# Performance work log

Hardware: AMD Instinct MI355X
Metric: run time of the kernel (lower is better)

The kernel has to match this reference:

```python
import jax, jax.numpy as jnp
import numpy as np

EPS = 1e-6


def setup_inputs() -> dict:
    key = jax.random.key(0)
    k1, k2, k3, k4 = jax.random.split(key, 4)
    B, L, H, E = 16, 4096, 8, 64
    return {
        "queries": jax.random.normal(k1, (B, L, H, E), dtype=jnp.float32),
        "keys": jax.random.normal(k2, (B, L, H, E), dtype=jnp.float32),
        "values": jax.random.normal(k3, (B, L, H, E), dtype=jnp.float32),
        "attn_mask": jnp.ones((1,), dtype=bool),
        "gamma": jax.random.uniform(k4, (1,), dtype=jnp.float32),
    }


def reference(queries, keys, values, attn_mask, gamma):
    # Faithful to the original: keys/values/attn_mask are unused; Q=K=V=queries.
    B, L, H, E = queries.shape
    HE = H * E
    V = queries.reshape(B, L, HE)              # raw values [B, L, HE]
    # l2_norm: normalize over dim=-2 (the L axis)
    Qn = V / jnp.linalg.norm(V, axis=-2, keepdims=True)   # [B, L, HE]
    Kt = jnp.swapaxes(Qn, -1, -2)              # K = l2_norm(K).permute -> [B, HE, L]
    # tailor_sum: 1 / (HE + sum_n Kt[b,n,l] * (sum_l' Qn[b,l',n] + eps))  -> [B, L]
    q_colsum = jnp.sum(Qn, axis=-2) + EPS      # [B, HE]
    tailor = 1.0 / (HE + jnp.einsum('bnl,bn->bl', Kt, q_colsum))  # [B, L]
    # value_sum over L, broadcast to [B, L, HE]
    value_sum = jnp.sum(V, axis=-2)            # [B, HE]
    # (V @ K) @ Q == V @ (K @ Q): use the linear-complexity [HE,HE] inner matrix
    KQ = jnp.einsum('bnl,blm->bnm', Kt, Qn)    # [B, HE, HE]
    part = jnp.einsum('bln,bnm->blm', V, KQ)   # [B, L, HE]
    matrix_sum = value_sum[:, None, :] + part  # [B, L, HE]
    weight_value = (matrix_sum * tailor[:, :, None]).reshape(B, L, H, E)
    return queries + gamma * weight_value
```

## Files before the change

### kernel.cpp

```cpp
#include <hip/hip_runtime.h>

#define EPS 1e-6f
#define LL 4096
#define HE 512

typedef __attribute__((ext_vector_type(8))) short short8;
typedef __attribute__((ext_vector_type(4))) float f32x4;

__device__ __forceinline__ unsigned short f2bf(float f) {
    union { float f; unsigned u; } v; v.f = f;
    unsigned r = v.u + 0x7FFFu + ((v.u >> 16) & 1u);
    return (unsigned short)(r >> 16);
}
__device__ __forceinline__ float bf2f(unsigned short s) {
    union { unsigned u; float f; } v; v.u = ((unsigned)s) << 16;
    return v.f;
}
__device__ __forceinline__ void gl16(const unsigned short* g, unsigned short* l) {
    __builtin_amdgcn_global_load_lds(
        (const __attribute__((address_space(1))) unsigned int*)(const void*)g,
        (__attribute__((address_space(3))) unsigned int*)(void*)l,
        16, 0, 0);
}

__global__ __launch_bounds__(256) void k1_fused(const float* __restrict__ q,
        unsigned short* __restrict__ Vt, unsigned short* __restrict__ Vb,
        float* __restrict__ ps, float* __restrict__ pq, int bofs, int pstride) {
    __shared__ unsigned short lds[64][65];
    int blk = blockIdx.x;
    int b = blk >> 9, lt = (blk >> 3) & 63, nt = blk & 7;
    int gb = bofs + b;
    int t = threadIdx.x;
    int row = t >> 4, col = (t & 15) << 2;
    const float* base = q + ((size_t)gb * LL + lt * 64) * HE + nt * 64;
    unsigned short* vbb = Vb + ((size_t)b * LL + lt * 64) * HE + nt * 64;
    #pragma unroll
    for (int i = 0; i < 4; i++) {
        int l = row + i * 16;
        float4 v = *(const float4*)(base + (size_t)l * HE + col);
        ushort4 w;
        w.x = f2bf(v.x); w.y = f2bf(v.y); w.z = f2bf(v.z); w.w = f2bf(v.w);
        lds[col+0][l] = w.x; lds[col+1][l] = w.y;
        lds[col+2][l] = w.z; lds[col+3][l] = w.w;
        *(ushort4*)(vbb + (size_t)l * HE + col) = w;
    }
    __syncthreads();
    unsigned short* ob = Vt + ((size_t)b * HE + nt * 64) * LL + lt * 64;
    #pragma unroll
    for (int i = 0; i < 4; i++) {
        int n = row + i * 16;
        ushort4 w;
        w.x = lds[n][col+0]; w.y = lds[n][col+1];
        w.z = lds[n][col+2]; w.w = lds[n][col+3];
        *(ushort4*)(ob + (size_t)n * LL + col) = w;
        float x0 = bf2f(w.x), x1 = bf2f(w.y), x2 = bf2f(w.z), x3 = bf2f(w.w);
        float s = x0 + x1 + x2 + x3;
        float qq = x0*x0 + x1*x1 + x2*x2 + x3*x3;
        s += __shfl_xor(s, 1);  qq += __shfl_xor(qq, 1);
        s += __shfl_xor(s, 2);  qq += __shfl_xor(qq, 2);
        s += __shfl_xor(s, 4);  qq += __shfl_xor(qq, 4);
        s += __shfl_xor(s, 8);  qq += __shfl_xor(qq, 8);
        if ((t & 15) == 0) {
            int idx = lt * pstride + b * 512 + nt * 64 + n;
            ps[idx] = s;
            pq[idx] = qq;
        }
    }
}

__global__ __launch_bounds__(256) void k2_reduce(const float* __restrict__ ps,
        const float* __restrict__ pq, float* __restrict__ sumV,
        float* __restrict__ cvec, float* __restrict__ invn, int bofs, int pstride) {
    int i = blockIdx.x * 256 + threadIdx.x;
    float s = 0.f, qq = 0.f;
    #pragma unroll 8
    for (int lt = 0; lt < 64; lt++) {
        s  += ps[(size_t)lt * pstride + i];
        qq += pq[(size_t)lt * pstride + i];
    }
    int o = bofs * HE + i;
    float inv = 1.0f / sqrtf(qq);
    sumV[o] = s;
    invn[o] = inv;
    cvec[o] = (s * inv + EPS) * inv;
}

__global__ __launch_bounds__(256) void k3_dvec(const unsigned short* __restrict__ Vb,
        const float* __restrict__ cvec, float* __restrict__ dvec, int bofs) {
    int blk = blockIdx.x;
    int b = blk >> 7, lblk = blk & 127;
    int t = threadIdx.x;
    int lloc = t >> 3, j = t & 7;
    int l = lblk * 32 + lloc;
    const unsigned short* rowp = Vb + ((size_t)b * LL + l) * HE + j * 64;
    const float* cp = cvec + (bofs + b) * HE + j * 64;
    float d = 0.f;
    #pragma unroll
    for (int g = 0; g < 8; g++) {
        short8 v = *(const short8*)(rowp + g * 8);
        float4 c0 = *(const float4*)(cp + g * 8);
        float4 c1 = *(const float4*)(cp + g * 8 + 4);
        d += bf2f((unsigned short)v[0]) * c0.x + bf2f((unsigned short)v[1]) * c0.y
           + bf2f((unsigned short)v[2]) * c0.z + bf2f((unsigned short)v[3]) * c0.w
           + bf2f((unsigned short)v[4]) * c1.x + bf2f((unsigned short)v[5]) * c1.y
           + bf2f((unsigned short)v[6]) * c1.z + bf2f((unsigned short)v[7]) * c1.w;
    }
    d += __shfl_xor(d, 1); d += __shfl_xor(d, 2); d += __shfl_xor(d, 4);
    if (j == 0) dvec[(size_t)(bofs + b) * LL + l] = d;
}

__global__ __launch_bounds__(256) void k4_gram(const unsigned short* __restrict__ Vt,
        unsigned short* __restrict__ Gp) {
    __shared__ __attribute__((aligned(16))) unsigned short la[128][64];
    __shared__ __attribute__((aligned(16))) unsigned short lb[128][64];
    int cpx = gridDim.x >> 3;
    int blk = ((int)blockIdx.x & 7) * cpx + ((int)blockIdx.x >> 3);
    int b = blk / 80;
    int rem = blk - b * 80;
    int pair = rem >> 3, split = rem & 7;
    int nt = (pair < 4) ? 0 : (pair < 7) ? 1 : (pair < 9) ? 2 : 3;
    int off = (nt * (9 - nt)) >> 1;
    int mt = nt + pair - off;
    bool diag = (nt == mt);
    int N0 = nt * 128, M0 = mt * 128;
    int t = threadIdx.x;
    int w = t >> 6, lane = t & 63;
    int wr = w >> 1, wc = w & 1;
    int rl = lane >> 3;
    int cl = ((lane & 7) ^ rl) << 3;
    int lr = lane & 15, q4 = lane >> 4;
    int ch0 = (q4 ^ (lane & 7)) << 3;
    const unsigned short* pa = Vt + ((size_t)b * HE + N0) * LL + split * 512;
    const unsigned short* pb = Vt + ((size_t)b * HE + M0) * LL + split * 512;
    const unsigned short (*LB)[64] = diag ? la : lb;
    f32x4 acc[4][4] = {};
    for (int kb = 0; kb < 8; kb++) {
        int k0 = kb * 64;
        #pragma unroll
        for (int p = 0; p < 4; p++) {
            int r0 = p * 32 + w * 8;
            gl16(pa + (size_t)(r0 + rl) * LL + k0 + cl, &la[r0][0]);
            if (!diag) gl16(pb + (size_t)(r0 + rl) * LL + k0 + cl, &lb[r0][0]);
        }
        __syncthreads();
        #pragma unroll
        for (int ks = 0; ks < 2; ks++) {
            int colA = ch0 ^ (ks << 5);
            short8 af[4], bfr[4];
            #pragma unroll
            for (int i = 0; i < 4; i++)
                af[i] = *(const short8*)&la[wr*64 + i*16 + lr][colA];
            #pragma unroll
            for (int j = 0; j < 4; j++)
                bfr[j] = *(const short8*)&LB[wc*64 + j*16 + lr][colA];
            #pragma unroll
            for (int i = 0; i < 4; i++)
                #pragma unroll
                for (int j = 0; j < 4; j++)
                    acc[i][j] = __builtin_amdgcn_mfma_f32_16x16x32_bf16(af[i], bfr[j], acc[i][j], 0, 0, 0);
        }
        __syncthreads();
    }
    size_t tbase = ((size_t)(b * 10 + pair) * 8 + split) * 16384;
    #pragma unroll
    for (int i = 0; i < 4; i++) {
        int nb = wr*64 + i*16 + q4*4;
        #pragma unroll
        for (int j = 0; j < 4; j++) {
            int ml = wc*64 + j*16 + lr;
            ushort4 wv;
            wv.x = f2bf(acc[i][j][0]); wv.y = f2bf(acc[i][j][1]);
            wv.z = f2bf(acc[i][j][2]); wv.w = f2bf(acc[i][j][3]);
            *(ushort4*)&Gp[tbase + (size_t)ml * 128 + nb] = wv;
        }
    }
}

__global__ __launch_bounds__(256) void k5_reduce(const unsigned short* __restrict__ Gp,
        const float* __restrict__ invn, unsigned short* __restrict__ KQb, int bofs) {
    __shared__ unsigned short lds_t[128][130];
    int blk = blockIdx.x;
    int b = blk / 10, pair = blk % 10;
    int nt = (pair < 4) ? 0 : (pair < 7) ? 1 : (pair < 9) ? 2 : 3;
    int off = (nt * (9 - nt)) >> 1;
    int mt = nt + pair - off;
    int N0 = nt * 128, M0 = mt * 128;
    int t = threadIdx.x;
    const unsigned short* gp = Gp + ((size_t)(b * 10 + pair) * 8) * 16384;
    const float* inb = invn + (size_t)(bofs + b) * HE;
    #pragma unroll 2
    for (int e = 0; e < 32; e++) {
        int idx = e * 512 + t * 2;
        int ml = idx >> 7, nl = idx & 127;
        float s0 = 0.f, s1 = 0.f;
        #pragma unroll
        for (int sp = 0; sp < 8; sp++) {
            unsigned g2 = *(const unsigned*)&gp[(size_t)sp * 16384 + idx];
            s0 += bf2f((unsigned short)(g2 & 0xFFFF));
            s1 += bf2f((unsigned short)(g2 >> 16));
        }
        float im = inb[M0 + ml];
        ushort2 v;
        v.x = f2bf(s0 * inb[N0 + nl] * im);
        v.y = f2bf(s1 * inb[N0 + nl + 1] * im);
        *(ushort2*)&KQb[((size_t)b * HE + M0 + ml) * HE + N0 + nl] = v;
        *(ushort2*)&lds_t[ml][nl] = v;
    }
    __syncthreads();
    #pragma unroll 2
    for (int e = 0; e < 32; e++) {
        int idx = e * 512 + t * 2;
        int nl = idx >> 7, ml = idx & 127;
        ushort2 v;
        v.x = lds_t[ml][nl];
        v.y = lds_t[ml + 1][nl];
        *(ushort2*)&KQb[((size_t)b * HE + N0 + nl) * HE + M0 + ml] = v;
    }
}

__global__ __launch_bounds__(256) void k6_part(const unsigned short* __restrict__ KQb,
        const unsigned short* __restrict__ Vb, const float* __restrict__ dvec,
        const float* __restrict__ sumV, const float* __restrict__ gamma,
        float* __restrict__ out, int bofs) {
    __shared__ __attribute__((aligned(16))) unsigned short la[128][64];
    __shared__ __attribute__((aligned(16))) unsigned short lb[128][64];
    int cpx = gridDim.x >> 3;
    int blk = ((int)blockIdx.x & 7) * cpx + ((int)blockIdx.x >> 3);
    int b = blk >> 7, mt = (blk >> 5) & 3, lt = blk & 31;
    int gb = bofs + b;
    int M0 = mt * 128, L0 = lt * 128;
    int t = threadIdx.x;
    int w = t >> 6, lane = t & 63;
    int wr = w >> 1, wc = w & 1;
    int rl = lane >> 3;
    int cl = ((lane & 7) ^ rl) << 3;
    int lr = lane & 15, q4 = lane >> 4;
    int ch0 = (q4 ^ (lane & 7)) << 3;
    const unsigned short* pa = KQb + ((size_t)b * HE + M0) * HE;
    const unsigned short* pb = Vb + ((size_t)b * LL + L0) * HE;
    f32x4 acc[4][4] = {};
    for (int kb = 0; kb < 8; kb++) {
        int k0 = kb * 64;
        #pragma unroll
        for (int p = 0; p < 4; p++) {
            int r0 = p * 32 + w * 8;
            gl16(pa + (size_t)(r0 + rl) * HE + k0 + cl, &la[r0][0]);
            gl16(pb + (size_t)(r0 + rl) * HE + k0 + cl, &lb[r0][0]);
        }
        __syncthreads();
        #pragma unroll
        for (int ks = 0; ks < 2; ks++) {
            int colA = ch0 ^ (ks << 5);
            short8 af[4], bfr[4];
            #pragma unroll
            for (int i = 0; i < 4; i++)
                af[i] = *(const short8*)&la[wr*64 + i*16 + lr][colA];
            #pragma unroll
            for (int j = 0; j < 4; j++)
                bfr[j] = *(const short8*)&lb[wc*64 + j*16 + lr][colA];
            #pragma unroll
            for (int i = 0; i < 4; i++)
                #pragma unroll
                for (int j = 0; j < 4; j++)
                    acc[i][j] = __builtin_amdgcn_mfma_f32_16x16x32_bf16(af[i], bfr[j], acc[i][j], 0, 0, 0);
        }
        __syncthreads();
    }
    float gma = gamma[0];
    #pragma unroll
    for (int j = 0; j < 4; j++) {
        int lglob = L0 + wc*64 + j*16 + lr;
        float dt = dvec[(size_t)gb * LL + lglob];
        float tailor = 1.0f / (512.0f + dt);
        #pragma unroll
        for (int i = 0; i < 4; i++) {
            int m4 = M0 + wr*64 + i*16 + q4*4;
            size_t ofs = ((size_t)gb * LL + lglob) * HE + m4;
            ushort4 rv = *(const ushort4*)(Vb + ((size_t)b * LL + lglob) * HE + m4);
            float4 vs = *(const float4*)(sumV + (size_t)gb * HE + m4);
            float4 o;
            o.x = bf2f(rv.x) + gma * (vs.x + acc[i][j][0]) * tailor;
            o.y = bf2f(rv.y) + gma * (vs.y + acc[i][j][1]) * tailor;
            o.z = bf2f(rv.z) + gma * (vs.z + acc[i][j][2]) * tailor;
            o.w = bf2f(rv.w) + gma * (vs.w + acc[i][j][3]) * tailor;
            *(float4*)(out + ofs) = o;
        }
    }
}

extern "C" void kernel_launch(void* const* d_in, const int* in_sizes, int n_in,
                              void* d_out, int out_size, void* d_ws, size_t ws_size,
                              hipStream_t stream) {
    const float* q     = (const float*)d_in[0];
    const float* gamma = (const float*)d_in[4];
    float* out = (float*)d_out;
    char* ws = (char*)d_ws;
    float* sumV  = (float*)(ws);
    float* cvec  = (float*)(ws + 65536);
    float* invn  = (float*)(ws + 98304);
    float* dvec  = (float*)(ws + 131072);

    if (ws_size >= 190000000ull) {
        unsigned short* KQb = (unsigned short*)(ws + 524288);
        unsigned short* Vt  = (unsigned short*)(ws + 8912896);
        unsigned short* Vb  = (unsigned short*)(ws + 76021760);
        unsigned short* Gp  = (unsigned short*)(ws + 143130624);
        float* ps = (float*)(ws + 185073664);
        float* pq = (float*)(ws + 187170816);
        k1_fused <<<8192, 256, 0, stream>>>(q, Vt, Vb, ps, pq, 0, 8192);
        k2_reduce<<<32,   256, 0, stream>>>(ps, pq, sumV, cvec, invn, 0, 8192);
        k3_dvec  <<<2048, 256, 0, stream>>>(Vb, cvec, dvec, 0);
        k4_gram  <<<1280, 256, 0, stream>>>(Vt, Gp);
        k5_reduce<<<160,  256, 0, stream>>>(Gp, invn, KQb, 0);
        k6_part  <<<2048, 256, 0, stream>>>(KQb, Vb, dvec, sumV, gamma, out, 0);
    } else {
        unsigned short* KQb = (unsigned short*)(ws + 524288);
        unsigned short* Vt  = (unsigned short*)(ws + 524288 + 4194304);
        unsigned short* Vb  = (unsigned short*)(ws + 524288 + 4194304 + 33554432);
        unsigned short* Gp = (unsigned short*)((float*)d_out + 16777216);
        float* ps = (float*)d_out + 22020096;
        float* pq = ps + 262144;
        for (int h = 0; h < 2; h++) {
            int bofs = h * 8;
            k1_fused <<<4096, 256, 0, stream>>>(q, Vt, Vb, ps, pq, bofs, 4096);
            k2_reduce<<<16,   256, 0, stream>>>(ps, pq, sumV, cvec, invn, bofs, 4096);
            k3_dvec  <<<1024, 256, 0, stream>>>(Vb, cvec, dvec, bofs);
            k4_gram  <<<640,  256, 0, stream>>>(Vt, Gp);
            k5_reduce<<<80,   256, 0, stream>>>(Gp, invn, KQb, bofs);
            k6_part  <<<1024, 256, 0, stream>>>(KQb, Vb, dvec, sumV, gamma, out, bofs);
        }
    }
}
```

Before: 210.5 us.

## Double-buffer LDS tiles in gram and part GEMM kernels

After: 199.5 us. 5.2% less time.

```diff
diff --git a/kernel.cpp b/kernel.cpp
--- a/kernel.cpp
+++ b/kernel.cpp
@@ -111,8 +111,8 @@
 
 __global__ __launch_bounds__(256) void k4_gram(const unsigned short* __restrict__ Vt,
         unsigned short* __restrict__ Gp) {
-    __shared__ __attribute__((aligned(16))) unsigned short la[128][64];
-    __shared__ __attribute__((aligned(16))) unsigned short lb[128][64];
+    __shared__ __attribute__((aligned(16))) unsigned short la[2][128][64];
+    __shared__ __attribute__((aligned(16))) unsigned short lb[2][128][64];
     int cpx = gridDim.x >> 3;
     int blk = ((int)blockIdx.x & 7) * cpx + ((int)blockIdx.x >> 3);
     int b = blk / 80;
@@ -132,35 +132,50 @@
     int ch0 = (q4 ^ (lane & 7)) << 3;
     const unsigned short* pa = Vt + ((size_t)b * HE + N0) * LL + split * 512;
     const unsigned short* pb = Vt + ((size_t)b * HE + M0) * LL + split * 512;
-    const unsigned short (*LB)[64] = diag ? la : lb;
     f32x4 acc[4][4] = {};
+
+#define STAGE4(B, KB) do { \
+    int _k0 = (KB) * 64; \
+    _Pragma("unroll") \
+    for (int p = 0; p < 4; p++) { \
+        int r0 = p * 32 + w * 8; \
+        gl16(pa + (size_t)(r0 + rl) * LL + _k0 + cl, &la[B][r0][0]); \
+        if (!diag) gl16(pb + (size_t)(r0 + rl) * LL + _k0 + cl, &lb[B][r0][0]); \
+    } } while (0)
+
+    STAGE4(0, 0);
+    #pragma unroll
     for (int kb = 0; kb < 8; kb++) {
-        int k0 = kb * 64;
-        #pragma unroll
-        for (int p = 0; p < 4; p++) {
-            int r0 = p * 32 + w * 8;
-            gl16(pa + (size_t)(r0 + rl) * LL + k0 + cl, &la[r0][0]);
-            if (!diag) gl16(pb + (size_t)(r0 + rl) * LL + k0 + cl, &lb[r0][0]);
-        }
-        __syncthreads();
+        int cur = kb & 1;
+        if (kb < 7) {
+            STAGE4(cur ^ 1, kb + 1);
+            if (diag) { asm volatile("s_waitcnt vmcnt(4)" ::: "memory"); }
+            else      { asm volatile("s_waitcnt vmcnt(8)" ::: "memory"); }
+        } else {
+            asm volatile("s_waitcnt vmcnt(0)" ::: "memory");
+        }
+        __builtin_amdgcn_s_barrier();
+        const unsigned short (*A)[64] = la[cur];
+        const unsigned short (*Bp)[64] = diag ? la[cur] : lb[cur];
         #pragma unroll
         for (int ks = 0; ks < 2; ks++) {
             int colA = ch0 ^ (ks << 5);
             short8 af[4], bfr[4];
             #pragma unroll
             for (int i = 0; i < 4; i++)
-                af[i] = *(const short8*)&la[wr*64 + i*16 + lr][colA];
+                af[i] = *(const short8*)&A[wr*64 + i*16 + lr][colA];
             #pragma unroll
             for (int j = 0; j < 4; j++)
-                bfr[j] = *(const short8*)&LB[wc*64 + j*16 + lr][colA];
+                bfr[j] = *(const short8*)&Bp[wc*64 + j*16 + lr][colA];
             #pragma unroll
             for (int i = 0; i < 4; i++)
                 #pragma unroll
                 for (int j = 0; j < 4; j++)
                     acc[i][j] = __builtin_amdgcn_mfma_f32_16x16x32_bf16(af[i], bfr[j], acc[i][j], 0, 0, 0);
         }
-        __syncthreads();
-    }
+        __builtin_amdgcn_s_barrier();
+    }
+#undef STAGE4
     size_t tbase = ((size_t)(b * 10 + pair) * 8 + split) * 16384;
     #pragma unroll
     for (int i = 0; i < 4; i++) {
@@ -222,8 +237,8 @@
         const unsigned short* __restrict__ Vb, const float* __restrict__ dvec,
         const float* __restrict__ sumV, const float* __restrict__ gamma,
         float* __restrict__ out, int bofs) {
-    __shared__ __attribute__((aligned(16))) unsigned short la[128][64];
-    __shared__ __attribute__((aligned(16))) unsigned short lb[128][64];
+    __shared__ __attribute__((aligned(16))) unsigned short la[2][128][64];
+    __shared__ __attribute__((aligned(16))) unsigned short lb[2][128][64];
     int cpx = gridDim.x >> 3;
     int blk = ((int)blockIdx.x & 7) * cpx + ((int)blockIdx.x >> 3);
     int b = blk >> 7, mt = (blk >> 5) & 3, lt = blk & 31;
@@ -238,35 +253,48 @@
     int ch0 = (q4 ^ (lane & 7)) << 3;
     const unsigned short* pa = KQb + ((size_t)b * HE + M0) * HE;
     const unsigned short* pb = Vb + ((size_t)b * LL + L0) * HE;
+    float gma = gamma[0];
     f32x4 acc[4][4] = {};
+
+#define STAGE6(B, KB) do { \
+    int _k0 = (KB) * 64; \
+    _Pragma("unroll") \
+    for (int p = 0; p < 4; p++) { \
+        int r0 = p * 32 + w * 8; \
+        gl16(pa + (size_t)(r0 + rl) * HE + _k0 + cl, &la[B][r0][0]); \
+        gl16(pb + (size_t)(r0 + rl) * HE + _k0 + cl, &lb[B][r0][0]); \
+    } } while (0)
+
+    STAGE6(0, 0);
+    #pragma unroll
     for (int kb = 0; kb < 8; kb++) {
-        int k0 = kb * 64;
-        #pragma unroll
-        for (int p = 0; p < 4; p++) {
-            int r0 = p * 32 + w * 8;
-            gl16(pa + (size_t)(r0 + rl) * HE + k0 + cl, &la[r0][0]);
-            gl16(pb + (size_t)(r0 + rl) * HE + k0 + cl, &lb[r0][0]);
-        }
-        __syncthreads();
+        int cur = kb & 1;
+        if (kb < 7) {
+            STAGE6(cur ^ 1, kb + 1);
+            asm volatile("s_waitcnt vmcnt(8)" ::: "memory");
+        } else {
+            asm volatile("s_waitcnt vmcnt(0)" ::: "memory");
+        }
+        __builtin_amdgcn_s_barrier();
         #pragma unroll
         for (int ks = 0; ks < 2; ks++) {
             int colA = ch0 ^ (ks << 5);
             short8 af[4], bfr[4];
             #pragma unroll
             for (int i = 0; i < 4; i++)
-                af[i] = *(const short8*)&la[wr*64 + i*16 + lr][colA];
+                af[i] = *(const short8*)&la[cur][wr*64 + i*16 + lr][colA];
             #pragma unroll
             for (int j = 0; j < 4; j++)
-                bfr[j] = *(const short8*)&lb[wc*64 + j*16 + lr][colA];
+                bfr[j] = *(const short8*)&lb[cur][wc*64 + j*16 + lr][colA];
             #pragma unroll
             for (int i = 0; i < 4; i++)
                 #pragma unroll
                 for (int j = 0; j < 4; j++)
                     acc[i][j] = __builtin_amdgcn_mfma_f32_16x16x32_bf16(af[i], bfr[j], acc[i][j], 0, 0, 0);
         }
-        __syncthreads();
-    }
-    float gma = gamma[0];
+        __builtin_amdgcn_s_barrier();
+    }
+#undef STAGE6
     #pragma unroll
     for (int j = 0; j < 4; j++) {
         int lglob = L0 + wc*64 + j*16 + lr;
```
